# Kernel optimization log

Hardware: AMD Instinct MI355X
Metric: run time of the kernel (lower is better)

Reference implementation:

```python
import jax, jax.numpy as jnp
import numpy as np

B, S, IN, N, MOT = 128, 4096, 6, 64, 3
ODE_UNFOLDS = 6
EPS = 1e-8


def setup_inputs() -> dict:
    ks = jax.random.split(jax.random.key(0), 20)
    u = lambda k, shape, lo, hi: jax.random.uniform(k, shape, jnp.float32, lo, hi)
    pm1 = lambda k, shape: jnp.where(jax.random.bernoulli(k, 0.5, shape), 1.0, -1.0).astype(jnp.float32)
    return {
        "x": jax.random.normal(ks[0], (B, S, IN), jnp.float32),
        "mean_us": 0.1 * jax.random.normal(ks[1], (IN,), jnp.float32),
        "std_us": u(ks[2], (IN,), 0.5, 1.5),
        "input_w": u(ks[3], (IN,), 0.8, 1.2),
        "input_b": 0.01 * jax.random.normal(ks[4], (IN,), jnp.float32),
        "output_w": u(ks[5], (MOT,), 0.8, 1.2),
        "output_b": 0.01 * jax.random.normal(ks[6], (MOT,), jnp.float32),
        "gleak": u(ks[7], (N,), 0.001, 1.0),
        "vleak": u(ks[8], (N,), -0.2, 0.2),
        "cm": u(ks[9], (N,), 0.4, 0.6),
        "sensory_W": u(ks[10], (IN, N), 0.001, 1.0),
        "sensory_mu": u(ks[11], (IN, N), 0.3, 0.8),
        "sensory_sigma": u(ks[12], (IN, N), 3.0, 8.0),
        "sensory_erev": pm1(ks[13], (IN, N)),
        "W": u(ks[14], (N, N), 0.001, 1.0),
        "mu": u(ks[15], (N, N), 0.3, 0.8),
        "sigma": u(ks[16], (N, N), 3.0, 8.0),
        "erev": pm1(ks[17], (N, N)),
    }


def _ltc_sequence(x, mean_us, std_us, input_w, input_b, output_w, output_b,
                  gleak, vleak, cm, sensory_W, sensory_mu, sensory_sigma,
                  sensory_erev, W, mu, sigma, erev):
    # normalize inputs (DgaRawSequence) then LTCCell input mapping
    xn = (x - mean_us) / std_us                      # [B,S,IN]
    xm = xn * input_w + input_b                      # [B,S,IN]
    cm_t = cm * ODE_UNFOLDS                          # cm / (elapsed_time=1 / ode_unfolds)

    def step(v, u_t):                                # v: [B,N], u_t: [B,IN]
        # sensory synapse activations [B,IN,N]
        s_act = sensory_W * jax.nn.sigmoid((u_t[:, :, None] - sensory_mu) * sensory_sigma)
        wns = jnp.sum(s_act * sensory_erev, axis=1)  # [B,N]
        wds = jnp.sum(s_act, axis=1)                 # [B,N]
        for _ in range(ODE_UNFOLDS):
            w_act = W * jax.nn.sigmoid((v[:, :, None] - mu) * sigma)  # [B,N,N]
            num = cm_t * v + gleak * vleak + jnp.sum(w_act * erev, axis=1) + wns
            den = cm_t + gleak + jnp.sum(w_act, axis=1) + wds
            v = num / (den + EPS)
        return v, v

    v0 = jnp.zeros((x.shape[0], gleak.shape[0]), dtype=x.dtype)
    _, vs = jax.lax.scan(step, v0, jnp.swapaxes(xm, 0, 1))   # [S,B,N]
    states = jnp.swapaxes(vs, 0, 1)                          # [B,S,N]
    # LTCCell output mapping (motor neurons = first MOT states)
    out = states[..., :MOT] * output_w + output_b            # [B,S,3]
    # denormalize (DgaRawSequence)
    return out * std_us[:MOT] + mean_us[:MOT]


def reference(x, mean_us, std_us, input_w, input_b, output_w, output_b,
              gleak, vleak, cm, sensory_W, sensory_mu, sensory_sigma,
              sensory_erev, W, mu, sigma, erev):
    return _ltc_sequence(x, mean_us, std_us, input_w, input_b, output_w,
                         output_b, gleak, vleak, cm, sensory_W, sensory_mu,
                         sensory_sigma, sensory_erev, W, mu, sigma, erev)
```

## Files before the change

### kernel.cpp

```cpp
#include <hip/hip_runtime.h>

#define B_ 128
#define S_ 4096
#define IN_ 6
#define N_ 64
#define MOT_ 3
#define UNF 6
#define EPS_ 1e-8f
#define LOG2E 1.4426950408889634f

typedef float v2f __attribute__((ext_vector_type(2)));

__device__ __forceinline__ float red16(float x) {
#if __has_builtin(__builtin_amdgcn_permlane16_swap)
    auto r = __builtin_amdgcn_permlane16_swap(__float_as_int(x), __float_as_int(x),
                                              false, false);
    return __int_as_float((int)r[0]) + __int_as_float((int)r[1]);
#else
    return x + __shfl_xor(x, 16, 64);
#endif
}
__device__ __forceinline__ float red32(float x) {
#if __has_builtin(__builtin_amdgcn_permlane32_swap)
    auto r = __builtin_amdgcn_permlane32_swap(__float_as_int(x), __float_as_int(x),
                                              false, false);
    return __int_as_float((int)r[0]) + __int_as_float((int)r[1]);
#else
    return x + __shfl_xor(x, 32, 64);
#endif
}

__device__ __forceinline__ void lds_barrier() {
    asm volatile("s_waitcnt lgkmcnt(0)" ::: "memory");
    __builtin_amdgcn_s_barrier();
}

__launch_bounds__(256, 1)
__global__ void ltc_kernel(
    const float* __restrict__ x,
    const float* __restrict__ mean_us, const float* __restrict__ std_us,
    const float* __restrict__ input_w, const float* __restrict__ input_b,
    const float* __restrict__ output_w, const float* __restrict__ output_b,
    const float* __restrict__ gleak, const float* __restrict__ vleak,
    const float* __restrict__ cm,
    const float* __restrict__ sW, const float* __restrict__ sMu,
    const float* __restrict__ sSig, const float* __restrict__ sErev,
    const float* __restrict__ W, const float* __restrict__ Mu,
    const float* __restrict__ Sig, const float* __restrict__ Erev,
    float* __restrict__ out)
{
    const int b    = blockIdx.x;
    const int t    = threadIdx.x;
    const int lane = t & 63;
    const int w    = t >> 6;
    const int cc   = lane >> 4;
    const int ii   = lane & 15;
    const int myCol = w * 16 + ii;
    const int jb   = cc * 16;

    __shared__ __align__(16) float vbuf[2][N_];

    v2f A2[8], B2[8];
    float Wr[16], We[16];
#pragma unroll
    for (int jj = 0; jj < 16; ++jj) {
        int idx = (jb + jj) * N_ + myCol;
        float sg = Sig[idx], m = Mu[idx], ww = W[idx], e = Erev[idx];
        A2[jj >> 1][jj & 1] = -sg * LOG2E;
        B2[jj >> 1][jj & 1] = m * sg * LOG2E;
        Wr[jj] = ww;
        We[jj] = ww * e;
    }

    const float cmt = cm[myCol] * (float)UNF;
    const float glk = gleak[myCol];
    const float gv  = glk * vleak[myCol];
    const float dbase = cmt + glk + EPS_;

    float SA[IN_], SB[IN_], SWe[IN_], SWv[IN_], NS[IN_], NB[IN_];
#pragma unroll
    for (int ci = 0; ci < IN_; ++ci) {
        int idx = ci * N_ + myCol;
        float sg = sSig[idx], m = sMu[idx], ww = sW[idx], e = sErev[idx];
        SA[ci]  = -sg * LOG2E;
        SB[ci]  = m * sg * LOG2E;
        SWv[ci] = ww;
        SWe[ci] = ww * e;
        NS[ci]  = input_w[ci] / std_us[ci];
        NB[ci]  = input_b[ci] - mean_us[ci] / std_us[ci] * input_w[ci];
    }

    float OW = 0.f, OB = 0.f;
    if (t < MOT_) {
        OW = output_w[t] * std_us[t];
        OB = output_b[t] * std_us[t] + mean_us[t];
    }

    const float* xb = x + (size_t)b * S_ * IN_;
    float* ob = out + (size_t)b * S_ * MOT_;

    if (t < N_) vbuf[0][t] = 0.f;

    float xc[IN_];
    {
        int off = 0;
        asm volatile("" : "+v"(off));
        float2 x01 = *(const float2*)(xb + off);
        float2 x23 = *(const float2*)(xb + off + 2);
        float2 x45 = *(const float2*)(xb + off + 4);
        xc[0] = x01.x; xc[1] = x01.y; xc[2] = x23.x;
        xc[3] = x23.y; xc[4] = x45.x; xc[5] = x45.y;
    }
    __syncthreads();

    float v_my = 0.f;

    for (int s = 0; s < S_; ++s) {
        const int s1 = (s + 1 < S_) ? (s + 1) : s;
        int off = s1 * IN_;
        asm volatile("" : "+v"(off));
        float2 p01 = *(const float2*)(xb + off);
        float2 p23 = *(const float2*)(xb + off + 2);
        float2 p45 = *(const float2*)(xb + off + 4);

        float wns = 0.f, wds = 0.f;
#pragma unroll
        for (int ci = 0; ci < IN_; ++ci) {
            float u  = fmaf(xc[ci], NS[ci], NB[ci]);
            float e  = __builtin_amdgcn_exp2f(fmaf(u, SA[ci], SB[ci]));
            float sg = __builtin_amdgcn_rcpf(1.0f + e);
            wns = fmaf(SWe[ci], sg, wns);
            wds = fmaf(SWv[ci], sg, wds);
        }
        const float nbs = gv + wns;
        const float dbs = dbase + wds;

#pragma unroll
        for (int k = 0; k < UNF; ++k) {
            const int p = k & 1;
            float4 q0 = *(const float4*)&vbuf[p][jb];
            float4 q1 = *(const float4*)&vbuf[p][jb + 4];
            float4 q2 = *(const float4*)&vbuf[p][jb + 8];
            float4 q3 = *(const float4*)&vbuf[p][jb + 12];
            const v2f vp[8] = {
                {q0.x, q0.y}, {q0.z, q0.w}, {q1.x, q1.y}, {q1.z, q1.w},
                {q2.x, q2.y}, {q2.z, q2.w}, {q3.x, q3.y}, {q3.z, q3.w}};

            float pn0 = 0.f, pd0 = 0.f, pn1 = 0.f, pd1 = 0.f;
#pragma unroll
            for (int pi = 0; pi < 8; ++pi) {
                v2f z  = __builtin_elementwise_fma(vp[pi], A2[pi], B2[pi]);
                v2f e  = {__builtin_amdgcn_exp2f(z.x), __builtin_amdgcn_exp2f(z.y)};
                v2f tt = e + 1.0f;
                float s0 = __builtin_amdgcn_rcpf(tt.x);
                float s1x = __builtin_amdgcn_rcpf(tt.y);
                pn0 = fmaf(We[2*pi],   s0,  pn0);
                pd0 = fmaf(Wr[2*pi],   s0,  pd0);
                pn1 = fmaf(We[2*pi+1], s1x, pn1);
                pd1 = fmaf(Wr[2*pi+1], s1x, pd1);
            }
            float pn = pn0 + pn1;
            float pd = pd0 + pd1;

            pn = red16(pn);  pd = red16(pd);
            pn = red32(pn);  pd = red32(pd);

            v_my = fmaf(cmt, v_my, nbs + pn) * __builtin_amdgcn_rcpf(dbs + pd);

            if (lane < 16) vbuf[p ^ 1][w * 16 + lane] = v_my;

            lds_barrier();
        }

        xc[0] = p01.x; xc[1] = p01.y; xc[2] = p23.x;
        xc[3] = p23.y; xc[4] = p45.x; xc[5] = p45.y;
        if (t < MOT_) ob[s * MOT_ + t] = fmaf(v_my, OW, OB);
    }
}

extern "C" void kernel_launch(void* const* d_in, const int* in_sizes, int n_in,
                              void* d_out, int out_size, void* d_ws, size_t ws_size,
                              hipStream_t stream) {
    (void)in_sizes; (void)n_in; (void)d_ws; (void)ws_size; (void)out_size;
    const float* x       = (const float*)d_in[0];
    const float* mean_us = (const float*)d_in[1];
    const float* std_us  = (const float*)d_in[2];
    const float* input_w = (const float*)d_in[3];
    const float* input_b = (const float*)d_in[4];
    const float* out_w   = (const float*)d_in[5];
    const float* out_b   = (const float*)d_in[6];
    const float* gleak   = (const float*)d_in[7];
    const float* vleak   = (const float*)d_in[8];
    const float* cm      = (const float*)d_in[9];
    const float* sW      = (const float*)d_in[10];
    const float* sMu     = (const float*)d_in[11];
    const float* sSig    = (const float*)d_in[12];
    const float* sErev   = (const float*)d_in[13];
    const float* W       = (const float*)d_in[14];
    const float* Mu      = (const float*)d_in[15];
    const float* Sig     = (const float*)d_in[16];
    const float* Erev    = (const float*)d_in[17];
    float* out = (float*)d_out;

    ltc_kernel<<<dim3(B_), dim3(256), 0, stream>>>(
        x, mean_us, std_us, input_w, input_b, out_w, out_b,
        gleak, vleak, cm, sW, sMu, sSig, sErev, W, Mu, Sig, Erev, out);
}
```

Before: 9.187 ms.

## Pack two batch sequences per 512-thread block sharing barriers

Each block now runs two independent batch sequences, each on four waves with its own LDS state buffer, so the grid shrinks from 128 to 64 blocks of 512 threads. The aim is to interleave two latency-bound recurrences on one CU so each hides the other's barrier and exp/rcp latency. The cost is that both sequences now wait on a shared block barrier. Also, only 64 of the device's CUs are occupied, which halves parallelism if blocks were previously spread one per CU.

```diff
diff --git a/kernel.cpp b/kernel.cpp
--- a/kernel.cpp
+++ b/kernel.cpp
@@ -35,7 +35,7 @@
     __builtin_amdgcn_s_barrier();
 }
 
-__launch_bounds__(256, 1)
+__launch_bounds__(512, 1)
 __global__ void ltc_kernel(
     const float* __restrict__ x,
     const float* __restrict__ mean_us, const float* __restrict__ std_us,
@@ -49,16 +49,17 @@
     const float* __restrict__ Sig, const float* __restrict__ Erev,
     float* __restrict__ out)
 {
-    const int b    = blockIdx.x;
     const int t    = threadIdx.x;
     const int lane = t & 63;
     const int w    = t >> 6;
+    const int ch   = w >> 2;
+    const int sw   = w & 3;
     const int cc   = lane >> 4;
     const int ii   = lane & 15;
-    const int myCol = w * 16 + ii;
+    const int myCol = sw * 16 + ii;
     const int jb   = cc * 16;
 
-    __shared__ __align__(16) float vbuf[2][N_];
+    __shared__ __align__(16) float vbuf[2][2][N_];
 
     v2f A2[8], B2[8];
     float Wr[16], We[16];
@@ -91,15 +92,16 @@
     }
 
     float OW = 0.f, OB = 0.f;
-    if (t < MOT_) {
-        OW = output_w[t] * std_us[t];
-        OB = output_b[t] * std_us[t] + mean_us[t];
-    }
-
+    if (myCol < MOT_) {
+        OW = output_w[myCol] * std_us[myCol];
+        OB = output_b[myCol] * std_us[myCol] + mean_us[myCol];
+    }
+
+    const int b = blockIdx.x * 2 + ch;
     const float* xb = x + (size_t)b * S_ * IN_;
     float* ob = out + (size_t)b * S_ * MOT_;
 
-    if (t < N_) vbuf[0][t] = 0.f;
+    if (lane < 16) vbuf[ch][0][sw * 16 + lane] = 0.f;
 
     float xc[IN_];
     {
@@ -138,10 +140,10 @@
 #pragma unroll
         for (int k = 0; k < UNF; ++k) {
             const int p = k & 1;
-            float4 q0 = *(const float4*)&vbuf[p][jb];
-            float4 q1 = *(const float4*)&vbuf[p][jb + 4];
-            float4 q2 = *(const float4*)&vbuf[p][jb + 8];
-            float4 q3 = *(const float4*)&vbuf[p][jb + 12];
+            float4 q0 = *(const float4*)&vbuf[ch][p][jb];
+            float4 q1 = *(const float4*)&vbuf[ch][p][jb + 4];
+            float4 q2 = *(const float4*)&vbuf[ch][p][jb + 8];
+            float4 q3 = *(const float4*)&vbuf[ch][p][jb + 12];
             const v2f vp[8] = {
                 {q0.x, q0.y}, {q0.z, q0.w}, {q1.x, q1.y}, {q1.z, q1.w},
                 {q2.x, q2.y}, {q2.z, q2.w}, {q3.x, q3.y}, {q3.z, q3.w}};
@@ -152,7 +154,7 @@
                 v2f z  = __builtin_elementwise_fma(vp[pi], A2[pi], B2[pi]);
                 v2f e  = {__builtin_amdgcn_exp2f(z.x), __builtin_amdgcn_exp2f(z.y)};
                 v2f tt = e + 1.0f;
-                float s0 = __builtin_amdgcn_rcpf(tt.x);
+                float s0  = __builtin_amdgcn_rcpf(tt.x);
                 float s1x = __builtin_amdgcn_rcpf(tt.y);
                 pn0 = fmaf(We[2*pi],   s0,  pn0);
                 pd0 = fmaf(Wr[2*pi],   s0,  pd0);
@@ -167,14 +169,14 @@
 
             v_my = fmaf(cmt, v_my, nbs + pn) * __builtin_amdgcn_rcpf(dbs + pd);
 
-            if (lane < 16) vbuf[p ^ 1][w * 16 + lane] = v_my;
+            if (lane < 16) vbuf[ch][p ^ 1][sw * 16 + lane] = v_my;
 
             lds_barrier();
         }
 
         xc[0] = p01.x; xc[1] = p01.y; xc[2] = p23.x;
         xc[3] = p23.y; xc[4] = p45.x; xc[5] = p45.y;
-        if (t < MOT_) ob[s * MOT_ + t] = fmaf(v_my, OW, OB);
+        if (sw == 0 && lane < MOT_) ob[s * MOT_ + lane] = fmaf(v_my, OW, OB);
     }
 }
 
@@ -202,7 +204,7 @@
     const float* Erev    = (const float*)d_in[17];
     float* out = (float*)d_out;
 
-    ltc_kernel<<<dim3(B_), dim3(256), 0, stream>>>(
+    ltc_kernel<<<dim3(B_ / 2), dim3(512), 0, stream>>>(
         x, mean_us, std_us, input_w, input_b, out_w, out_b,
         gleak, vleak, cm, sW, sMu, sSig, sErev, W, Mu, Sig, Erev, out);
 }
```

Result: slower. 15.21 ms (+65.6%).

## Get own-wave neuron states via ds_bpermute and read other waves' from LDS

Applied to the files above, without the earlier changes.

Permutes the row assignment so that each wave's first quad of presynaptic neurons is its own 16 outputs. Those four values now come through ds_bpermute of the freshly computed v_my instead of an LDS round trip, and only three float4 LDS reads remain per unfold. The cmt*v+nbs term is also precomputed ahead of the reduction to shorten the dependent chain. The trade-off is extra bpermute instructions per unfold, and the barrier is still required for the cross-wave data.

```diff
diff --git a/kernel.cpp b/kernel.cpp
--- a/kernel.cpp
+++ b/kernel.cpp
@@ -28,6 +28,10 @@
 #else
     return x + __shfl_xor(x, 32, 64);
 #endif
+}
+
+__device__ __forceinline__ float bperm(int addr, float v) {
+    return __int_as_float(__builtin_amdgcn_ds_bpermute(addr, __float_as_int(v)));
 }
 
 __device__ __forceinline__ void lds_barrier() {
@@ -55,21 +59,27 @@
     const int w    = t >> 6;
     const int cc   = lane >> 4;
     const int ii   = lane & 15;
-    const int myCol = w * 16 + ii;
-    const int jb   = cc * 16;
+    const int myCol = (w << 4) + ii;
+    const int cc4  = cc << 2;
 
     __shared__ __align__(16) float vbuf[2][N_];
 
     v2f A2[8], B2[8];
     float Wr[16], We[16];
 #pragma unroll
-    for (int jj = 0; jj < 16; ++jj) {
-        int idx = (jb + jj) * N_ + myCol;
-        float sg = Sig[idx], m = Mu[idx], ww = W[idx], e = Erev[idx];
-        A2[jj >> 1][jj & 1] = -sg * LOG2E;
-        B2[jj >> 1][jj & 1] = m * sg * LOG2E;
-        Wr[jj] = ww;
-        We[jj] = ww * e;
+    for (int d = 0; d < 4; ++d) {
+        const int q  = (w + d) & 3;
+        const int j0 = (q << 4) + cc4;
+#pragma unroll
+        for (int r = 0; r < 4; ++r) {
+            int idx = (j0 + r) * N_ + myCol;
+            float sg = Sig[idx], m = Mu[idx], ww = W[idx], e = Erev[idx];
+            const int mm = 4 * d + r;
+            A2[mm >> 1][mm & 1] = -sg * LOG2E;
+            B2[mm >> 1][mm & 1] = m * sg * LOG2E;
+            Wr[mm] = ww;
+            We[mm] = ww * e;
+        }
     }
 
     const float cmt = cm[myCol] * (float)UNF;
@@ -99,7 +109,14 @@
     const float* xb = x + (size_t)b * S_ * IN_;
     float* ob = out + (size_t)b * S_ * MOT_;
 
-    if (t < N_) vbuf[0][t] = 0.f;
+    if (lane < 16) vbuf[0][(w << 4) + lane] = 0.f;
+    float ov0 = 0.f, ov1 = 0.f, ov2 = 0.f, ov3 = 0.f;
+
+    const int bp0 = (cc4 + 0) << 2, bp1 = (cc4 + 1) << 2;
+    const int bp2 = (cc4 + 2) << 2, bp3 = (cc4 + 3) << 2;
+    const int ro1 = (((w + 1) & 3) << 4) + cc4;
+    const int ro2 = (((w + 2) & 3) << 4) + cc4;
+    const int ro3 = (((w + 3) & 3) << 4) + cc4;
 
     float xc[IN_];
     {
@@ -134,40 +151,67 @@
         }
         const float nbs = gv + wns;
         const float dbs = dbase + wds;
+        float cv = fmaf(cmt, v_my, nbs);
 
 #pragma unroll
         for (int k = 0; k < UNF; ++k) {
             const int p = k & 1;
-            float4 q0 = *(const float4*)&vbuf[p][jb];
-            float4 q1 = *(const float4*)&vbuf[p][jb + 4];
-            float4 q2 = *(const float4*)&vbuf[p][jb + 8];
-            float4 q3 = *(const float4*)&vbuf[p][jb + 12];
-            const v2f vp[8] = {
-                {q0.x, q0.y}, {q0.z, q0.w}, {q1.x, q1.y}, {q1.z, q1.w},
-                {q2.x, q2.y}, {q2.z, q2.w}, {q3.x, q3.y}, {q3.z, q3.w}};
-
-            float pn0 = 0.f, pd0 = 0.f, pn1 = 0.f, pd1 = 0.f;
-#pragma unroll
-            for (int pi = 0; pi < 8; ++pi) {
-                v2f z  = __builtin_elementwise_fma(vp[pi], A2[pi], B2[pi]);
-                v2f e  = {__builtin_amdgcn_exp2f(z.x), __builtin_amdgcn_exp2f(z.y)};
-                v2f tt = e + 1.0f;
-                float s0 = __builtin_amdgcn_rcpf(tt.x);
-                float s1x = __builtin_amdgcn_rcpf(tt.y);
-                pn0 = fmaf(We[2*pi],   s0,  pn0);
-                pd0 = fmaf(Wr[2*pi],   s0,  pd0);
-                pn1 = fmaf(We[2*pi+1], s1x, pn1);
-                pd1 = fmaf(Wr[2*pi+1], s1x, pd1);
+            float4 r1 = *(const float4*)&vbuf[p][ro1];
+            float4 r2 = *(const float4*)&vbuf[p][ro2];
+            float4 r3 = *(const float4*)&vbuf[p][ro3];
+
+            float pn0, pd0, pn1, pd1, pn2, pd2, pn3, pd3;
+            {
+                v2f z0 = __builtin_elementwise_fma((v2f){ov0, ov1}, A2[0], B2[0]);
+                v2f z1 = __builtin_elementwise_fma((v2f){ov2, ov3}, A2[1], B2[1]);
+                v2f t0 = {__builtin_amdgcn_exp2f(z0.x), __builtin_amdgcn_exp2f(z0.y)};
+                v2f t1 = {__builtin_amdgcn_exp2f(z1.x), __builtin_amdgcn_exp2f(z1.y)};
+                t0 = t0 + 1.0f;  t1 = t1 + 1.0f;
+                float s0 = __builtin_amdgcn_rcpf(t0.x);
+                float s1x = __builtin_amdgcn_rcpf(t0.y);
+                float s2 = __builtin_amdgcn_rcpf(t1.x);
+                float s3 = __builtin_amdgcn_rcpf(t1.y);
+                pn0 = fmaf(We[0], s0, fmaf(We[1], s1x, fmaf(We[2], s2, We[3] * s3)));
+                pd0 = fmaf(Wr[0], s0, fmaf(Wr[1], s1x, fmaf(Wr[2], s2, Wr[3] * s3)));
             }
-            float pn = pn0 + pn1;
-            float pd = pd0 + pd1;
+#define QUAD(D, RV, PN, PD)                                                     \
+            {                                                                   \
+                v2f z0 = __builtin_elementwise_fma((v2f){RV.x, RV.y},           \
+                                                   A2[2*(D)], B2[2*(D)]);       \
+                v2f z1 = __builtin_elementwise_fma((v2f){RV.z, RV.w},           \
+                                                   A2[2*(D)+1], B2[2*(D)+1]);   \
+                v2f t0 = {__builtin_amdgcn_exp2f(z0.x),                         \
+                          __builtin_amdgcn_exp2f(z0.y)};                        \
+                v2f t1 = {__builtin_amdgcn_exp2f(z1.x),                         \
+                          __builtin_amdgcn_exp2f(z1.y)};                        \
+                t0 = t0 + 1.0f;  t1 = t1 + 1.0f;                                \
+                float s0 = __builtin_amdgcn_rcpf(t0.x);                         \
+                float s1x = __builtin_amdgcn_rcpf(t0.y);                        \
+                float s2 = __builtin_amdgcn_rcpf(t1.x);                         \
+                float s3 = __builtin_amdgcn_rcpf(t1.y);                         \
+                PN = fmaf(We[4*(D)], s0, fmaf(We[4*(D)+1], s1x,                 \
+                     fmaf(We[4*(D)+2], s2, We[4*(D)+3] * s3)));                 \
+                PD = fmaf(Wr[4*(D)], s0, fmaf(Wr[4*(D)+1], s1x,                 \
+                     fmaf(Wr[4*(D)+2], s2, Wr[4*(D)+3] * s3)));                 \
+            }
+            QUAD(1, r1, pn1, pd1)
+            QUAD(2, r2, pn2, pd2)
+            QUAD(3, r3, pn3, pd3)
+#undef QUAD
+            float pn = (pn0 + pn1) + (pn2 + pn3);
+            float pd = (pd0 + pd1) + (pd2 + pd3);
 
             pn = red16(pn);  pd = red16(pd);
             pn = red32(pn);  pd = red32(pd);
 
-            v_my = fmaf(cmt, v_my, nbs + pn) * __builtin_amdgcn_rcpf(dbs + pd);
-
-            if (lane < 16) vbuf[p ^ 1][w * 16 + lane] = v_my;
+            v_my = (cv + pn) * __builtin_amdgcn_rcpf(dbs + pd);
+
+            if (lane < 16) vbuf[p ^ 1][(w << 4) + lane] = v_my;
+            ov0 = bperm(bp0, v_my);
+            ov1 = bperm(bp1, v_my);
+            ov2 = bperm(bp2, v_my);
+            ov3 = bperm(bp3, v_my);
+            cv  = fmaf(cmt, v_my, nbs);
 
             lds_barrier();
         }
```

After: 9.918 ms. 1.08x slower.
